# Kernel optimization log

Measured on AMD Instinct MI355X. Metric: run time of the kernel, lower is better.

## Reference

```python
import jax, jax.numpy as jnp
import numpy as np
from jax.ops import segment_sum

N_NODES = 50000


def gcn_conv(x, src, dst, W, b, n_nodes):
    # PyG GCNConv with default add_self_loops=True, normalize=True.
    # deg includes self-loops (weight 1 each).
    deg = segment_sum(jnp.ones_like(dst, dtype=x.dtype), dst, num_segments=n_nodes) + 1.0
    dinv = jax.lax.rsqrt(deg)  # [N]
    h = x @ W                  # [N, out]
    # messages over real edges: norm[src]*norm[dst]*h[src]
    msg = h[src] * (dinv[src] * dinv[dst])[:, None]   # [E, out]
    agg = segment_sum(msg, dst, num_segments=n_nodes)  # [N, out]
    # self-loop contribution: dinv[i]^2 * h[i]
    agg = agg + h * (dinv * dinv)[:, None]
    return agg + b


def setup_inputs() -> dict:
    key = jax.random.key(0)
    k1, k2, k3, k4 = jax.random.split(key, 4)
    N, E, d_in, d_hid, d_out = N_NODES, 800000, 128, 128, 64
    x = jax.random.normal(k1, (N, d_in), dtype=jnp.float32)
    edge_index = jax.random.randint(k2, (2, E), 0, N, dtype=jnp.int64)
    W1 = jax.random.normal(k3, (d_in, d_hid), dtype=jnp.float32) / np.sqrt(d_in)
    b1 = jnp.zeros((d_hid,), dtype=jnp.float32)
    W2 = jax.random.normal(k4, (d_hid, d_out), dtype=jnp.float32) / np.sqrt(d_hid)
    b2 = jnp.zeros((d_out,), dtype=jnp.float32)
    return {"x": x, "edge_index": edge_index, "W1": W1, "b1": b1, "W2": W2, "b2": b2}


def reference(x, edge_index, W1, b1, W2, b2):
    src, dst = edge_index[0], edge_index[1]
    h = gcn_conv(x, src, dst, W1, b1, N_NODES)
    h = jax.nn.relu(h)
    out = gcn_conv(h, src, dst, W2, b2, N_NODES)
    return out
```

## Files before the change

kernel.cpp:

```cpp
#include <hip/hip_runtime.h>
#include <hip/hip_bf16.h>


#define ELL_CAP 64

typedef __attribute__((ext_vector_type(8))) short short8;
typedef __attribute__((ext_vector_type(4))) float f32x4;

static __device__ __forceinline__ unsigned short f2bf(float f) {
    unsigned int u = __float_as_uint(f);
    u = (u + 0x7fff + ((u >> 16) & 1)) >> 16;
    return (unsigned short)u;
}
static __device__ __forceinline__ float2 bfunpack(unsigned int u) {
    return make_float2(__uint_as_float(u << 16),
                       __uint_as_float(u & 0xffff0000u));
}


__global__ void zero_cnt(int* __restrict__ cnt, int n) {
    int i = blockIdx.x * blockDim.x + threadIdx.x;
    if (i < n) cnt[i] = 0;
}

__global__ void build_ell(const int* __restrict__ src, const int* __restrict__ dst,
                          int* __restrict__ cnt, int* __restrict__ ell, int E) {
    int e = blockIdx.x * blockDim.x + threadIdx.x;
    if (e >= E) return;
    int d = dst[e];
    int pos = atomicAdd(&cnt[d], 1);
    if (pos < ELL_CAP) ell[(size_t)d * ELL_CAP + pos] = src[e];
}

__global__ void compute_dinv(const int* __restrict__ cnt, float* __restrict__ dinv, int n) {
    int i = blockIdx.x * blockDim.x + threadIdx.x;
    if (i < n) dinv[i] = rsqrtf((float)cnt[i] + 1.0f);
}

__global__ void f32_to_bf16_vec(const float* __restrict__ in, unsigned short* __restrict__ out, int n4) {
    int i = blockIdx.x * blockDim.x + threadIdx.x;
    if (i >= n4) return;
    float4 v = ((const float4*)in)[i];
    ushort4 o;
    o.x = f2bf(v.x); o.y = f2bf(v.y); o.z = f2bf(v.z); o.w = f2bf(v.w);
    ((ushort4*)out)[i] = o;
}

__global__ void transpose_w_bf16(const float* __restrict__ w, short* __restrict__ wt, int ncols) {
    int i = blockIdx.x * blockDim.x + threadIdx.x;
    if (i >= 128 * ncols) return;
    int k = i / ncols, nn = i % ncols;
    wt[nn * 128 + k] = (short)f2bf(w[i]);
}


template<int NC>
__global__ __launch_bounds__(256) void gemm_mfma(
    const short* __restrict__ A, const short* __restrict__ Bt,
    const float* __restrict__ dinv, unsigned short* __restrict__ Cb, int n)
{
    __shared__ short Bs[NC][136];
    const int tid = threadIdx.x;

    #pragma unroll
    for (int i = 0; i < NC / 16; ++i) {
        int idx = tid + i * 256;
        int nrow = idx >> 4;
        int kcol = (idx & 15) * 8;
        *(short8*)&Bs[nrow][kcol] = *(const short8*)(Bt + nrow * 128 + kcol);
    }
    __syncthreads();

    const int wave = tid >> 6, lane = tid & 63;
    const int row0 = blockIdx.x * 64 + wave * 16;
    if (row0 >= n) return;
    const int quad = lane >> 4, l16 = lane & 15;

    short8 af[4];
    const short* arow = A + (size_t)(row0 + l16) * 128 + quad * 8;
    #pragma unroll
    for (int kk = 0; kk < 4; ++kk)
        af[kk] = *(const short8*)(arow + kk * 32);

    float dv[4];
    #pragma unroll
    for (int r = 0; r < 4; ++r) dv[r] = dinv[row0 + quad * 4 + r];

    #pragma unroll
    for (int t = 0; t < NC / 16; ++t) {
        f32x4 acc = {0.f, 0.f, 0.f, 0.f};
        #pragma unroll
        for (int kk = 0; kk < 4; ++kk) {
            short8 bfr = *(const short8*)&Bs[t * 16 + l16][kk * 32 + quad * 8];
            acc = __builtin_amdgcn_mfma_f32_16x16x32_bf16(af[kk], bfr, acc, 0, 0, 0);
        }
        #pragma unroll
        for (int r = 0; r < 4; ++r) {
            int gr = row0 + quad * 4 + r;
            Cb[(size_t)gr * NC + t * 16 + l16] = f2bf(acc[r] * dv[r]);
        }
    }
}


__global__ __launch_bounds__(256) void aggregate_l1(
    const unsigned int* __restrict__ hp, const int* __restrict__ ell,
    const int* __restrict__ cnt, const float* __restrict__ dinv,
    const float* __restrict__ bias, unsigned int* __restrict__ z1b, int n)
{
    int node = blockIdx.x * 4 + (threadIdx.x >> 6);
    if (node >= n) return;
    int lane = threadIdx.x & 63;
    int deg = cnt[node];
    if (deg > ELL_CAP) deg = ELL_CAP;
    const int* __restrict__ row = ell + (size_t)node * ELL_CAP;
    float d = dinv[node];

    float2 acc = bfunpack(hp[(size_t)node * 64 + lane]);
    int e = 0;
    for (; e + 4 <= deg; e += 4) {
        int s0 = row[e], s1 = row[e + 1], s2 = row[e + 2], s3 = row[e + 3];
        float2 v0 = bfunpack(hp[(size_t)s0 * 64 + lane]);
        float2 v1 = bfunpack(hp[(size_t)s1 * 64 + lane]);
        float2 v2 = bfunpack(hp[(size_t)s2 * 64 + lane]);
        float2 v3 = bfunpack(hp[(size_t)s3 * 64 + lane]);
        acc.x += (v0.x + v1.x) + (v2.x + v3.x);
        acc.y += (v0.y + v1.y) + (v2.y + v3.y);
    }
    for (; e < deg; ++e) {
        float2 v = bfunpack(hp[(size_t)row[e] * 64 + lane]);
        acc.x += v.x; acc.y += v.y;
    }
    float ox = fmaxf(fmaf(acc.x, d, bias[lane * 2]), 0.f);
    float oy = fmaxf(fmaf(acc.y, d, bias[lane * 2 + 1]), 0.f);
    z1b[(size_t)node * 64 + lane] =
        (unsigned int)f2bf(ox) | ((unsigned int)f2bf(oy) << 16);
}


__global__ __launch_bounds__(256) void aggregate_l2(
    const unsigned int* __restrict__ hp, const int* __restrict__ ell,
    const int* __restrict__ cnt, const float* __restrict__ dinv,
    const float* __restrict__ bias, float* __restrict__ out, int n)
{
    int lane = threadIdx.x & 63;
    int half = lane >> 5, l32 = lane & 31;
    int node = blockIdx.x * 8 + (threadIdx.x >> 6) * 2 + half;
    if (node >= n) return;
    int deg = cnt[node];
    if (deg > ELL_CAP) deg = ELL_CAP;
    const int* __restrict__ row = ell + (size_t)node * ELL_CAP;
    float d = dinv[node];

    float2 acc = bfunpack(hp[(size_t)node * 32 + l32]);
    int e = 0;
    for (; e + 4 <= deg; e += 4) {
        int s0 = row[e], s1 = row[e + 1], s2 = row[e + 2], s3 = row[e + 3];
        float2 v0 = bfunpack(hp[(size_t)s0 * 32 + l32]);
        float2 v1 = bfunpack(hp[(size_t)s1 * 32 + l32]);
        float2 v2 = bfunpack(hp[(size_t)s2 * 32 + l32]);
        float2 v3 = bfunpack(hp[(size_t)s3 * 32 + l32]);
        acc.x += (v0.x + v1.x) + (v2.x + v3.x);
        acc.y += (v0.y + v1.y) + (v2.y + v3.y);
    }
    for (; e < deg; ++e) {
        float2 v = bfunpack(hp[(size_t)row[e] * 32 + l32]);
        acc.x += v.x; acc.y += v.y;
    }
    float2 o;
    o.x = fmaf(acc.x, d, bias[l32 * 2]);
    o.y = fmaf(acc.y, d, bias[l32 * 2 + 1]);
    ((float2*)out)[(size_t)node * 32 + l32] = o;
}


extern "C" void kernel_launch(void* const* d_in, const int* in_sizes, int n_in,
                              void* d_out, int out_size, void* d_ws, size_t ws_size,
                              hipStream_t stream)
{
    const float* x  = (const float*)d_in[0];
    const int*   ei = (const int*)d_in[1];
    const float* W1 = (const float*)d_in[2];
    const float* b1 = (const float*)d_in[3];
    const float* W2 = (const float*)d_in[4];
    const float* b2 = (const float*)d_in[5];
    float* out = (float*)d_out;

    const int N = in_sizes[0] / 128;
    const int E = in_sizes[1] / 2;
    const int* src = ei;
    const int* dst = ei + E;

    char* ws = (char*)d_ws;
    size_t off = 0;
    auto alloc = [&](size_t bytes) -> void* {
        void* p = ws + off;
        off += (bytes + 255) & ~(size_t)255;
        return p;
    };
    int*            cnt  = (int*)           alloc((size_t)N * 4);
    float*          dinv = (float*)         alloc((size_t)N * 4);
    int*            ell  = (int*)           alloc((size_t)N * ELL_CAP * 4);
    unsigned short* xb   = (unsigned short*)alloc((size_t)N * 128 * 2);
    short*          w1t  = (short*)         alloc((size_t)128 * 128 * 2);
    short*          w2t  = (short*)         alloc((size_t)64 * 128 * 2);
    unsigned short* h1b  = (unsigned short*)alloc((size_t)N * 128 * 2);
    unsigned int*   z1b  = (unsigned int*)  alloc((size_t)N * 64 * 4);
    unsigned short* h2b  = (unsigned short*)alloc((size_t)N * 64 * 2);

    zero_cnt    <<<(N + 255) / 256, 256, 0, stream>>>(cnt, N);
    build_ell   <<<(E + 255) / 256, 256, 0, stream>>>(src, dst, cnt, ell, E);
    compute_dinv<<<(N + 255) / 256, 256, 0, stream>>>(cnt, dinv, N);

    f32_to_bf16_vec<<<(N * 128 / 4 + 255) / 256, 256, 0, stream>>>(x, xb, N * 128 / 4);
    transpose_w_bf16<<<(128 * 128 + 255) / 256, 256, 0, stream>>>(W1, w1t, 128);
    transpose_w_bf16<<<(128 * 64 + 255) / 256, 256, 0, stream>>>(W2, w2t, 64);

    gemm_mfma<128><<<(N + 63) / 64, 256, 0, stream>>>((const short*)xb, w1t, dinv, h1b, N);
    aggregate_l1<<<(N + 3) / 4, 256, 0, stream>>>((const unsigned int*)h1b, ell, cnt, dinv, b1, z1b, N);

    gemm_mfma<64><<<(N + 63) / 64, 256, 0, stream>>>((const short*)z1b, w2t, dinv, h2b, N);
    aggregate_l2<<<(N + 7) / 8, 256, 0, stream>>>((const unsigned int*)h2b, ell, cnt, dinv, b2, out, N);
}
```

Before: 210.3 us.

## Partition ELL build by destination range and fuse input conversions into GEMM

Replaces the single-pass ELL build with a destination-partitioned version. Each of 8 partitions rescans the edge list but only does atomics and scatters for its node range, which improves the locality of those atomics and writes. The separate x-to-bf16 conversion kernel is folded into the first GEMM's A-load, and the two weight transposes are merged into one launch. The dinv array is dropped and rsqrt is recomputed from cnt in each consumer. The trade-off is that the edge indices are read 8 times, in exchange for fewer launches and no round trip through an intermediate bf16 copy of x.

New measurement: 197.3 us. 1.07x faster.

```diff
diff --git a/kernel.cpp b/kernel.cpp
--- a/kernel.cpp
+++ b/kernel.cpp
@@ -3,6 +3,7 @@
 
 
 #define ELL_CAP 64
+#define NPART 8
 
 typedef __attribute__((ext_vector_type(8))) short short8;
 typedef __attribute__((ext_vector_type(4))) float f32x4;
@@ -23,41 +24,44 @@
     if (i < n) cnt[i] = 0;
 }
 
-__global__ void build_ell(const int* __restrict__ src, const int* __restrict__ dst,
-                          int* __restrict__ cnt, int* __restrict__ ell, int E) {
-    int e = blockIdx.x * blockDim.x + threadIdx.x;
-    if (e >= E) return;
-    int d = dst[e];
-    int pos = atomicAdd(&cnt[d], 1);
-    if (pos < ELL_CAP) ell[(size_t)d * ELL_CAP + pos] = src[e];
-}
-
-__global__ void compute_dinv(const int* __restrict__ cnt, float* __restrict__ dinv, int n) {
+__global__ __launch_bounds__(256) void build_ell_part(
+    const int* __restrict__ src, const int* __restrict__ dst,
+    int* __restrict__ cnt, int* __restrict__ ell, int E, int partSize)
+{
+    const int part   = blockIdx.x & (NPART - 1);
+    const int chunk  = blockIdx.x >> 3;
+    const int nchunk = gridDim.x >> 3;
+    const int lo = part * partSize, hi = lo + partSize;
+    const int per = (E + nchunk - 1) / nchunk;
+    const int e1 = min((chunk + 1) * per, E);
+    for (int e = chunk * per + threadIdx.x; e < e1; e += 256) {
+        int d = dst[e];
+        if (d >= lo && d < hi) {
+            int pos = atomicAdd(&cnt[d], 1);
+            if (pos < ELL_CAP) ell[(size_t)d * ELL_CAP + pos] = src[e];
+        }
+    }
+}
+
+__global__ void convert_weights(const float* __restrict__ W1, const float* __restrict__ W2,
+                                short* __restrict__ w1t, short* __restrict__ w2t)
+{
     int i = blockIdx.x * blockDim.x + threadIdx.x;
-    if (i < n) dinv[i] = rsqrtf((float)cnt[i] + 1.0f);
-}
-
-__global__ void f32_to_bf16_vec(const float* __restrict__ in, unsigned short* __restrict__ out, int n4) {
-    int i = blockIdx.x * blockDim.x + threadIdx.x;
-    if (i >= n4) return;
-    float4 v = ((const float4*)in)[i];
-    ushort4 o;
-    o.x = f2bf(v.x); o.y = f2bf(v.y); o.z = f2bf(v.z); o.w = f2bf(v.w);
-    ((ushort4*)out)[i] = o;
-}
-
-__global__ void transpose_w_bf16(const float* __restrict__ w, short* __restrict__ wt, int ncols) {
-    int i = blockIdx.x * blockDim.x + threadIdx.x;
-    if (i >= 128 * ncols) return;
-    int k = i / ncols, nn = i % ncols;
-    wt[nn * 128 + k] = (short)f2bf(w[i]);
-}
-
-
-template<int NC>
+    if (i < 128 * 128) {
+        int k = i >> 7, nn = i & 127;
+        w1t[nn * 128 + k] = (short)f2bf(W1[i]);
+    } else if (i < 128 * 128 + 128 * 64) {
+        int j = i - 128 * 128;
+        int k = j >> 6, nn = j & 63;
+        w2t[nn * 128 + k] = (short)f2bf(W2[j]);
+    }
+}
+
+
+template<int NC, bool AF32>
 __global__ __launch_bounds__(256) void gemm_mfma(
-    const short* __restrict__ A, const short* __restrict__ Bt,
-    const float* __restrict__ dinv, unsigned short* __restrict__ Cb, int n)
+    const void* __restrict__ Av, const short* __restrict__ Bt,
+    const int* __restrict__ cnt, unsigned short* __restrict__ Cb, int n)
 {
     __shared__ short Bs[NC][136];
     const int tid = threadIdx.x;
@@ -77,14 +81,30 @@
     const int quad = lane >> 4, l16 = lane & 15;
 
     short8 af[4];
-    const short* arow = A + (size_t)(row0 + l16) * 128 + quad * 8;
-    #pragma unroll
-    for (int kk = 0; kk < 4; ++kk)
-        af[kk] = *(const short8*)(arow + kk * 32);
+    if (AF32) {
+        const float* arow = (const float*)Av + (size_t)(row0 + l16) * 128 + quad * 8;
+        #pragma unroll
+        for (int kk = 0; kk < 4; ++kk) {
+            float4 u = *(const float4*)(arow + kk * 32);
+            float4 v = *(const float4*)(arow + kk * 32 + 4);
+            short8 f;
+            f[0] = (short)f2bf(u.x); f[1] = (short)f2bf(u.y);
+            f[2] = (short)f2bf(u.z); f[3] = (short)f2bf(u.w);
+            f[4] = (short)f2bf(v.x); f[5] = (short)f2bf(v.y);
+            f[6] = (short)f2bf(v.z); f[7] = (short)f2bf(v.w);
+            af[kk] = f;
+        }
+    } else {
+        const short* arow = (const short*)Av + (size_t)(row0 + l16) * 128 + quad * 8;
+        #pragma unroll
+        for (int kk = 0; kk < 4; ++kk)
+            af[kk] = *(const short8*)(arow + kk * 32);
+    }
 
     float dv[4];
     #pragma unroll
-    for (int r = 0; r < 4; ++r) dv[r] = dinv[row0 + quad * 4 + r];
+    for (int r = 0; r < 4; ++r)
+        dv[r] = rsqrtf((float)cnt[row0 + quad * 4 + r] + 1.0f);
 
     #pragma unroll
     for (int t = 0; t < NC / 16; ++t) {
@@ -105,16 +125,16 @@
 
 __global__ __launch_bounds__(256) void aggregate_l1(
     const unsigned int* __restrict__ hp, const int* __restrict__ ell,
-    const int* __restrict__ cnt, const float* __restrict__ dinv,
-    const float* __restrict__ bias, unsigned int* __restrict__ z1b, int n)
+    const int* __restrict__ cnt, const float* __restrict__ bias,
+    unsigned int* __restrict__ z1b, int n)
 {
     int node = blockIdx.x * 4 + (threadIdx.x >> 6);
     if (node >= n) return;
     int lane = threadIdx.x & 63;
     int deg = cnt[node];
+    float d = rsqrtf((float)deg + 1.0f);
     if (deg > ELL_CAP) deg = ELL_CAP;
     const int* __restrict__ row = ell + (size_t)node * ELL_CAP;
-    float d = dinv[node];
 
     float2 acc = bfunpack(hp[(size_t)node * 64 + lane]);
     int e = 0;
@@ -140,17 +160,17 @@
 
 __global__ __launch_bounds__(256) void aggregate_l2(
     const unsigned int* __restrict__ hp, const int* __restrict__ ell,
-    const int* __restrict__ cnt, const float* __restrict__ dinv,
-    const float* __restrict__ bias, float* __restrict__ out, int n)
+    const int* __restrict__ cnt, const float* __restrict__ bias,
+    float* __restrict__ out, int n)
 {
     int lane = threadIdx.x & 63;
     int half = lane >> 5, l32 = lane & 31;
     int node = blockIdx.x * 8 + (threadIdx.x >> 6) * 2 + half;
     if (node >= n) return;
     int deg = cnt[node];
+    float d = rsqrtf((float)deg + 1.0f);
     if (deg > ELL_CAP) deg = ELL_CAP;
     const int* __restrict__ row = ell + (size_t)node * ELL_CAP;
-    float d = dinv[node];
 
     float2 acc = bfunpack(hp[(size_t)node * 32 + l32]);
     int e = 0;
@@ -190,6 +210,7 @@
     const int E = in_sizes[1] / 2;
     const int* src = ei;
     const int* dst = ei + E;
+    const int partSize = (N + NPART - 1) / NPART;
 
     char* ws = (char*)d_ws;
     size_t off = 0;
@@ -199,26 +220,20 @@
         return p;
     };
     int*            cnt  = (int*)           alloc((size_t)N * 4);
-    float*          dinv = (float*)         alloc((size_t)N * 4);
     int*            ell  = (int*)           alloc((size_t)N * ELL_CAP * 4);
-    unsigned short* xb   = (unsigned short*)alloc((size_t)N * 128 * 2);
     short*          w1t  = (short*)         alloc((size_t)128 * 128 * 2);
     short*          w2t  = (short*)         alloc((size_t)64 * 128 * 2);
     unsigned short* h1b  = (unsigned short*)alloc((size_t)N * 128 * 2);
     unsigned int*   z1b  = (unsigned int*)  alloc((size_t)N * 64 * 4);
     unsigned short* h2b  = (unsigned short*)alloc((size_t)N * 64 * 2);
 
-    zero_cnt    <<<(N + 255) / 256, 256, 0, stream>>>(cnt, N);
-    build_ell   <<<(E + 255) / 256, 256, 0, stream>>>(src, dst, cnt, ell, E);
-    compute_dinv<<<(N + 255) / 256, 256, 0, stream>>>(cnt, dinv, N);
-
-    f32_to_bf16_vec<<<(N * 128 / 4 + 255) / 256, 256, 0, stream>>>(x, xb, N * 128 / 4);
-    transpose_w_bf16<<<(128 * 128 + 255) / 256, 256, 0, stream>>>(W1, w1t, 128);
-    transpose_w_bf16<<<(128 * 64 + 255) / 256, 256, 0, stream>>>(W2, w2t, 64);
-
-    gemm_mfma<128><<<(N + 63) / 64, 256, 0, stream>>>((const short*)xb, w1t, dinv, h1b, N);
-    aggregate_l1<<<(N + 3) / 4, 256, 0, stream>>>((const unsigned int*)h1b, ell, cnt, dinv, b1, z1b, N);
-
-    gemm_mfma<64><<<(N + 63) / 64, 256, 0, stream>>>((const short*)z1b, w2t, dinv, h2b, N);
-    aggregate_l2<<<(N + 7) / 8, 256, 0, stream>>>((const unsigned int*)h2b, ell, cnt, dinv, b2, out, N);
-}
+    convert_weights<<<(128 * 192 + 255) / 256, 256, 0, stream>>>(W1, W2, w1t, w2t);
+    zero_cnt<<<(N + 255) / 256, 256, 0, stream>>>(cnt, N);
+    build_ell_part<<<128 * NPART, 256, 0, stream>>>(src, dst, cnt, ell, E, partSize);
+
+    gemm_mfma<128, true><<<(N + 63) / 64, 256, 0, stream>>>(x, w1t, cnt, h1b, N);
+    aggregate_l1<<<(N + 3) / 4, 256, 0, stream>>>((const unsigned int*)h1b, ell, cnt, b1, z1b, N);
+
+    gemm_mfma<64, false><<<(N + 63) / 64, 256, 0, stream>>>(z1b, w2t, cnt, h2b, N);
+    aggregate_l2<<<(N + 7) / 8, 256, 0, stream>>>((const unsigned int*)h2b, ell, cnt, b2, out, N);
+}
```
